# Kernel tuning notes

Hardware: AMD Instinct MI355X
Metric: run time of the kernel (lower is better)

The kernel has to match this reference:

```python
import jax, jax.numpy as jnp
import numpy as np

V, D, F, H, L = 32000, 1024, 4096, 16, 6
HD = D // H
EPS = 1e-5


def _posenc(S):
    pos = jnp.arange(S, dtype=jnp.float32)[:, None]
    div = jnp.exp(jnp.arange(0, D, 2, dtype=jnp.float32) * (-jnp.log(10000.0) / D))
    enc = jnp.zeros((S, D), jnp.float32)
    enc = enc.at[:, 0::2].set(jnp.sin(pos * div))
    enc = enc.at[:, 1::2].set(jnp.cos(pos * div))
    return enc


def _mha(xq, xkv, Wq, bq, Wk, bk, Wv, bv, Wo, bo, causal):
    B, Sq, _ = xq.shape
    Sk = xkv.shape[1]
    q = (xq @ Wq.T + bq).reshape(B, Sq, H, HD)
    k = (xkv @ Wk.T + bk).reshape(B, Sk, H, HD)
    v = (xkv @ Wv.T + bv).reshape(B, Sk, H, HD)
    scores = jnp.einsum('bqhd,bkhd->bhqk', q, k) / jnp.sqrt(jnp.float32(HD))
    if causal:
        mask = jnp.tril(jnp.ones((Sq, Sk), dtype=bool))
        scores = jnp.where(mask, scores, -jnp.inf)
    w = jax.nn.softmax(scores, axis=-1)
    out = jnp.einsum('bhqk,bkhd->bqhd', w, v).reshape(B, Sq, D)
    return out @ Wo.T + bo


def _ln(x, g, b):
    mu = jnp.mean(x, axis=-1, keepdims=True)
    var = jnp.mean((x - mu) ** 2, axis=-1, keepdims=True)
    return (x - mu) / jnp.sqrt(var + EPS) * g + b


def setup_inputs() -> dict:
    key = jax.random.key(0)
    ks = jax.random.split(key, 32)
    B, S, Se = 4, 512, 512
    s = 0.02
    inp = {
        'text': jax.random.randint(ks[0], (B, S), 0, V),
        'encoder_output': jax.random.normal(ks[1], (B, Se, D), jnp.float32),
        'W_e': jax.random.normal(ks[2], (V, D), jnp.float32) * s,
        'b_out': jnp.zeros((V,), jnp.float32),
        'ln_g': jnp.ones((D,), jnp.float32),
        'ln_b': jnp.zeros((D,), jnp.float32),
        'W1': jax.random.normal(ks[3], (F, D), jnp.float32) * s,
        'b1': jnp.zeros((F,), jnp.float32),
        'W2': jax.random.normal(ks[4], (D, F), jnp.float32) * s,
        'b2': jnp.zeros((D,), jnp.float32),
    }
    names = ['mWq', 'mWk', 'mWv', 'mWo', 'cWq', 'cWk', 'cWv', 'cWo']
    for i, n in enumerate(names):
        inp[n] = jax.random.normal(ks[5 + i], (D, D), jnp.float32) * s
        inp[n.replace('W', 'b')] = jnp.zeros((D,), jnp.float32)
    return inp


def reference(text, encoder_output, W_e, b_out, ln_g, ln_b, W1, b1, W2, b2,
              mWq, mbq, mWk, mbk, mWv, mbv, mWo, mbo,
              cWq, cbq, cWk, cbk, cWv, cbv, cWo, cbo):
    # embed + sinusoidal positional encoding (dropout is identity in eval)
    x = W_e[text] + _posenc(text.shape[1])[None, :, :]
    # NOTE: the torch module reuses the SAME attention/FFN/LN weights each layer
    for _ in range(L):
        a = _ln(x + _mha(x, x, mWq, mbq, mWk, mbk, mWv, mbv, mWo, mbo, True), ln_g, ln_b)
        c = _ln(_mha(a, encoder_output, cWq, cbq, cWk, cbk, cWv, cbv, cWo, cbo, False) + a, ln_g, ln_b)
        f = jax.nn.relu(c @ W1.T + b1) @ W2.T + b2
        x = _ln(c + f, ln_g, ln_b)
    logits = x @ W_e.T + b_out  # tied embedding weights
    # nn.Softmax() with dim=None on a 3-D tensor -> torch legacy dim=0
    return jax.nn.softmax(logits, axis=0)
```

## Files before the change

kernel.cpp:

```cpp
#include <hip/hip_runtime.h>

#define D_MODEL 1024
#define SEQ     512
#define NBATCH  4
#define NHEAD   16
#define HDIM    64
#define NTOK    2048
#define VOCAB   32000
#define FFDIM   4096
#define MiB     (1024*1024)

typedef _Float16 f16;
typedef f16   f16x8 __attribute__((ext_vector_type(8)));
typedef float f32x4 __attribute__((ext_vector_type(4)));

__device__ __forceinline__ void async_cp16(f16* lds, const f16* g) {
    __builtin_amdgcn_global_load_lds(
        (const __attribute__((address_space(1))) unsigned int*)g,
        (__attribute__((address_space(3))) unsigned int*)lds, 16, 0, 0);
}

__device__ __forceinline__ float block_sum(float v, float* lds) {
    #pragma unroll
    for (int o = 1; o < 64; o <<= 1) v += __shfl_xor(v, o);
    int w = threadIdx.x >> 6;
    if ((threadIdx.x & 63) == 0) lds[w] = v;
    __syncthreads();
    v = lds[0] + lds[1] + lds[2] + lds[3];
    __syncthreads();
    return v;
}

__global__ __launch_bounds__(256) void f32_to_f16_kernel(
    const float* __restrict__ in, f16* __restrict__ out, int n)
{
    int i0 = blockIdx.x * 1024 + threadIdx.x;
    #pragma unroll
    for (int e = 0; e < 4; e++) {
        int i = i0 + e * 256;
        if (i < n) out[i] = (f16)in[i];
    }
}

__global__ __launch_bounds__(256) void embed_kernel(
    const int* __restrict__ text, const float* __restrict__ We,
    float* __restrict__ X, f16* __restrict__ X16)
{
    int s = blockIdx.x;
    int tid = threadIdx.x;
    int tok[NBATCH];
    #pragma unroll
    for (int b = 0; b < NBATCH; b++) tok[b] = text[b * SEQ + s];
    const float kf = 9.210340371976184f / 1024.f;
    #pragma unroll
    for (int e = 0; e < 4; e++) {
        int d = tid + e * 256;
        int i2 = d & ~1;
        float freq = expf(-(float)i2 * kf);
        float ang = (float)s * freq;
        float pe = (d & 1) ? cosf(ang) : sinf(ang);
        #pragma unroll
        for (int b = 0; b < NBATCH; b++) {
            float v = We[(size_t)tok[b] * D_MODEL + d] + pe;
            size_t off = (size_t)(b * SEQ + s) * D_MODEL + d;
            X[off] = v;
            X16[off] = (f16)v;
        }
    }
}

template<bool RELU, int OUTMODE, int BM, bool QKV3>
__global__ __launch_bounds__(256) void gemm16_kernel(
    const f16* __restrict__ A, const f16* __restrict__ W,
    const float* __restrict__ bias, const float* __restrict__ bias2,
    const float* __restrict__ bias3,
    float* __restrict__ C, f16* __restrict__ C16, int M, int N, int K)
{
    constexpr int AM = BM / 2;
    constexpr int TM = AM / 16;
    __shared__ __align__(16) f16 As[BM * 32];
    __shared__ __align__(16) f16 Bs[128 * 32];
    const int tid  = threadIdx.x;
    const int lane = tid & 63;
    const int wv   = tid >> 6;
    const int wr   = (wv >> 1) * AM;
    const int wc   = (wv & 1) * 64;
    const int m0 = blockIdx.y * BM;
    const int n0 = blockIdx.x * 128;
    const int lm = lane & 15;
    const int lk = (lane >> 4) * 8;

    f32x4 acc[TM][4] = {};

    for (int k0 = 0; k0 < K; k0 += 32) {
        #pragma unroll
        for (int e = 0; e < BM / 64; e++) {
            int s = tid + e * 256;
            int row = s >> 2, cb = s & 3;
            async_cp16(&As[s * 8], &A[(size_t)(m0 + row) * K + k0 + cb * 8]);
        }
        #pragma unroll
        for (int e = 0; e < 2; e++) {
            int s = tid + e * 256;
            int row = s >> 2, cb = s & 3;
            async_cp16(&Bs[s * 8], &W[(size_t)(n0 + row) * K + k0 + cb * 8]);
        }
        __syncthreads();
        f16x8 af[TM], bfr[4];
        #pragma unroll
        for (int i = 0; i < TM; i++)
            af[i]  = *(const f16x8*)&As[(wr + i * 16 + lm) * 32 + lk];
        #pragma unroll
        for (int j = 0; j < 4; j++)
            bfr[j] = *(const f16x8*)&Bs[(wc + j * 16 + lm) * 32 + lk];
        #pragma unroll
        for (int i = 0; i < TM; i++)
            #pragma unroll
            for (int j = 0; j < 4; j++)
                acc[i][j] = __builtin_amdgcn_mfma_f32_16x16x32_f16(
                    af[i], bfr[j], acc[i][j], 0, 0, 0);
        __syncthreads();
    }

    const int rq = (lane >> 4) * 4;
    #pragma unroll
    for (int i = 0; i < TM; i++) {
        #pragma unroll
        for (int j = 0; j < 4; j++) {
            int col = n0 + wc + j * 16 + lm;
            float bj;
            if (QKV3) {
                const float* bp = col < 1024 ? bias : (col < 2048 ? bias2 : bias3);
                bj = bp[col & 1023];
            } else {
                bj = bias[col];
            }
            if (OUTMODE == 2) {
                int srow = (m0 + wr + i * 16 + rq) >> 2;
                float v[4];
                float mx = -1e30f;
                #pragma unroll
                for (int r = 0; r < 4; r++) {
                    v[r] = acc[i][j][r] + bj;
                    mx = fmaxf(mx, v[r]);
                }
                float ssum = 0.f;
                #pragma unroll
                for (int r = 0; r < 4; r++) { v[r] = expf(v[r] - mx); ssum += v[r]; }
                float inv = 1.f / ssum;
                #pragma unroll
                for (int r = 0; r < 4; r++)
                    C[((size_t)r * SEQ + srow) * N + col] = v[r] * inv;
            } else {
                #pragma unroll
                for (int r = 0; r < 4; r++) {
                    int row = m0 + wr + i * 16 + rq + r;
                    float v = acc[i][j][r] + bj;
                    if (RELU) v = fmaxf(v, 0.f);
                    if (OUTMODE == 0) C[(size_t)row * N + col] = v;
                    else              C16[(size_t)row * N + col] = (f16)v;
                }
            }
        }
    }
}

template<int CAUSAL>
__global__ __launch_bounds__(256) void attn_sm_kernel(
    const f16* __restrict__ Qb, const f16* __restrict__ Kb,
    f16* __restrict__ P, int ldq, int ldk, int qoff, int koff)
{
    __shared__ __align__(16) f16 Qs[2][64][32];
    __shared__ __align__(16) f16 Ks[2][2][128][32];
    const int bh = blockIdx.y;
    const int b = bh >> 4, h = bh & 15;
    const int q0 = blockIdx.x * 64;
    const int tid  = threadIdx.x;
    const int lane = tid & 63;
    const int w    = tid >> 6;
    const int lm   = lane & 15;
    const int lk   = (lane >> 4) * 8;
    const int nkt  = CAUSAL ? (q0 >> 7) + 1 : 4;
    const int nj   = nkt * 8;

    const f16* Qg = Qb + (size_t)(b * SEQ + q0) * ldq + qoff + h * HDIM;
    const f16* Kg = Kb + (size_t)(b * SEQ) * ldk + koff + h * HDIM;

    #pragma unroll
    for (int e = 0; e < 2; e++) {
        int cc = tid + e * 256;
        int ks = cc >> 8, row = (cc >> 2) & 63, cb = cc & 3;
        async_cp16(&Qs[ks][row][cb * 8], &Qg[(size_t)row * ldq + ks * 32 + cb * 8]);
    }
    #pragma unroll
    for (int e = 0; e < 4; e++) {
        int cc = tid + e * 256;
        int ks = cc >> 9, row = (cc >> 2) & 127, cb = cc & 3;
        async_cp16(&Ks[0][ks][row][cb * 8], &Kg[(size_t)row * ldk + ks * 32 + cb * 8]);
    }
    __syncthreads();

    f16x8 af[2];
    af[0] = *(const f16x8*)&Qs[0][w * 16 + lm][lk];
    af[1] = *(const f16x8*)&Qs[1][w * 16 + lm][lk];

    f32x4 acc[32] = {};

    #pragma unroll
    for (int kt = 0; kt < 4; kt++) {
        if (kt < nkt) {
            if (kt + 1 < nkt) {
                const f16* src = Kg + (size_t)(kt + 1) * 128 * ldk;
                int buf = (kt + 1) & 1;
                #pragma unroll
                for (int e = 0; e < 4; e++) {
                    int cc = tid + e * 256;
                    int ks = cc >> 9, row = (cc >> 2) & 127, cb = cc & 3;
                    async_cp16(&Ks[buf][ks][row][cb * 8],
                               &src[(size_t)row * ldk + ks * 32 + cb * 8]);
                }
            }
            #pragma unroll
            for (int ks = 0; ks < 2; ks++)
                #pragma unroll
                for (int j = 0; j < 8; j++) {
                    f16x8 bf = *(const f16x8*)&Ks[kt & 1][ks][j * 16 + lm][lk];
                    acc[kt * 8 + j] = __builtin_amdgcn_mfma_f32_16x16x32_f16(
                        af[ks], bf, acc[kt * 8 + j], 0, 0, 0);
                }
            if (kt + 1 < nkt) __syncthreads();
        }
    }

    const int rq = (lane >> 4) * 4;
    #pragma unroll
    for (int r = 0; r < 4; r++) {
        const int qq = q0 + w * 16 + rq + r;
        float mr = -1e30f;
        #pragma unroll
        for (int j = 0; j < 32; j++) {
            if (j < nj) {
                float v = acc[j][r] * 0.125f;
                if (CAUSAL && (j * 16 + lm) > qq) v = -1e30f;
                acc[j][r] = v;
                mr = fmaxf(mr, v);
            }
        }
        mr = fmaxf(mr, __shfl_xor(mr, 1));
        mr = fmaxf(mr, __shfl_xor(mr, 2));
        mr = fmaxf(mr, __shfl_xor(mr, 4));
        mr = fmaxf(mr, __shfl_xor(mr, 8));
        float sum = 0.f;
        #pragma unroll
        for (int j = 0; j < 32; j++) {
            if (j < nj) {
                float e = expf(acc[j][r] - mr);
                acc[j][r] = e;
                sum += e;
            }
        }
        sum += __shfl_xor(sum, 1);
        sum += __shfl_xor(sum, 2);
        sum += __shfl_xor(sum, 4);
        sum += __shfl_xor(sum, 8);
        float inv = 1.f / sum;
        f16* prow = P + ((size_t)bh * SEQ + qq) * SEQ + lm;
        #pragma unroll
        for (int j = 0; j < 32; j++) {
            float pv = (j < nj) ? acc[j][r] * inv : 0.f;
            prow[j * 16] = (f16)pv;
        }
    }
}

__global__ __launch_bounds__(256) void attn_av16_kernel(
    const f16* __restrict__ P, const f16* __restrict__ Vt,
    f16* __restrict__ O16, int causal)
{
    __shared__ __align__(16) f16 Ps[64 * 32];
    __shared__ __align__(16) f16 Vs[64 * 32];
    const int bh = blockIdx.y;
    const int b = bh >> 4, h = bh & 15;
    const int q0 = blockIdx.x * 64;
    const int tid  = threadIdx.x;
    const int lane = tid & 63;
    const int wv   = tid >> 6;
    const int wr   = (wv >> 1) * 32;
    const int wc   = (wv & 1) * 32;
    const int lm   = lane & 15;
    const int lk   = (lane >> 4) * 8;
    const f16* Pg = P  + ((size_t)bh * SEQ + q0) * SEQ;
    const f16* Vg = Vt + (size_t)bh * HDIM * SEQ;
    const int klim = causal ? q0 + 64 : SEQ;

    f32x4 acc[2][2] = {};
    for (int k0 = 0; k0 < klim; k0 += 32) {
        int row = tid >> 2, cb = tid & 3;
        async_cp16(&Ps[tid * 8], &Pg[(size_t)row * SEQ + k0 + cb * 8]);
        async_cp16(&Vs[tid * 8], &Vg[(size_t)row * SEQ + k0 + cb * 8]);
        __syncthreads();
        f16x8 af[2], bf[2];
        #pragma unroll
        for (int i = 0; i < 2; i++)
            af[i] = *(const f16x8*)&Ps[(wr + i * 16 + lm) * 32 + lk];
        #pragma unroll
        for (int j = 0; j < 2; j++)
            bf[j] = *(const f16x8*)&Vs[(wc + j * 16 + lm) * 32 + lk];
        #pragma unroll
        for (int i = 0; i < 2; i++)
            #pragma unroll
            for (int j = 0; j < 2; j++)
                acc[i][j] = __builtin_amdgcn_mfma_f32_16x16x32_f16(
                    af[i], bf[j], acc[i][j], 0, 0, 0);
        __syncthreads();
    }

    const int rq = (lane >> 4) * 4;
    #pragma unroll
    for (int i = 0; i < 2; i++)
        #pragma unroll
        for (int j = 0; j < 2; j++)
            #pragma unroll
            for (int r = 0; r < 4; r++)
                O16[(size_t)(b * SEQ + q0 + wr + i * 16 + rq + r) * D_MODEL
                    + h * HDIM + wc + j * 16 + lm] = (f16)acc[i][j][r];
}

__global__ __launch_bounds__(256) void vtrans_kernel(
    const f16* __restrict__ V, f16* __restrict__ Vt, int ldv, int vbase)
{
    __shared__ __align__(16) f16 t[64][72];
    const int bh = blockIdx.y;
    const int b = bh >> 4, h = bh & 15;
    const int s0 = blockIdx.x * 64;
    const int tid = threadIdx.x;
    const int r = tid >> 3;
    const int c8 = (tid & 7) * 8;
    #pragma unroll
    for (int half = 0; half < 2; half++) {
        int row = r + half * 32;
        f16x8 v = *(const f16x8*)&V[(size_t)(b * SEQ + s0 + row) * ldv
                                    + vbase + h * HDIM + c8];
        #pragma unroll
        for (int j = 0; j < 8; j++) t[c8 + j][row] = v[j];
    }
    __syncthreads();
    const int d = tid >> 2;
    const int sblk = (tid & 3) * 16;
    f16* dst = Vt + ((size_t)bh * HDIM + d) * SEQ + s0 + sblk;
    *(f16x8*)&dst[0] = *(const f16x8*)&t[d][sblk];
    *(f16x8*)&dst[8] = *(const f16x8*)&t[d][sblk + 8];
}

template<bool IL>
__global__ __launch_bounds__(256) void add_ln_kernel(
    const float* __restrict__ X, const float* __restrict__ Y,
    const float* __restrict__ g, const float* __restrict__ bb,
    float* __restrict__ Out, f16* __restrict__ Out16)
{
    __shared__ float lds[4];
    int row = blockIdx.x;
    const float* xp = X + (size_t)row * D_MODEL;
    const float* yp = Y + (size_t)row * D_MODEL;
    int tid = threadIdx.x;
    float s[4];
    float lsum = 0.f;
    #pragma unroll
    for (int e = 0; e < 4; e++) {
        int d = tid + e * 256;
        s[e] = xp[d] + yp[d];
        lsum += s[e];
    }
    float mu = block_sum(lsum, lds) * (1.f / D_MODEL);
    float lv = 0.f;
    #pragma unroll
    for (int e = 0; e < 4; e++) { float t = s[e] - mu; lv += t * t; }
    float rstd = rsqrtf(block_sum(lv, lds) * (1.f / D_MODEL) + 1e-5f);
    int orow = IL ? ((row & (SEQ - 1)) * 4 + (row >> 9)) : row;
    #pragma unroll
    for (int e = 0; e < 4; e++) {
        int d = tid + e * 256;
        float v = (s[e] - mu) * rstd * g[d] + bb[d];
        Out[(size_t)row * D_MODEL + d] = v;
        Out16[(size_t)orow * D_MODEL + d] = (f16)v;
    }
}

extern "C" void kernel_launch(void* const* d_in, const int* in_sizes, int n_in,
                              void* d_out, int out_size, void* d_ws, size_t ws_size,
                              hipStream_t stream)
{
    const int*   text = (const int*)d_in[0];
    const float* enc  = (const float*)d_in[1];
    const float* W_e  = (const float*)d_in[2];
    const float* b_out= (const float*)d_in[3];
    const float* ln_g = (const float*)d_in[4];
    const float* ln_b = (const float*)d_in[5];
    const float* W1   = (const float*)d_in[6];
    const float* b1   = (const float*)d_in[7];
    const float* W2   = (const float*)d_in[8];
    const float* b2   = (const float*)d_in[9];
    const float* mWq  = (const float*)d_in[10]; const float* mbq = (const float*)d_in[11];
    const float* mWk  = (const float*)d_in[12]; const float* mbk = (const float*)d_in[13];
    const float* mWv  = (const float*)d_in[14]; const float* mbv = (const float*)d_in[15];
    const float* mWo  = (const float*)d_in[16]; const float* mbo = (const float*)d_in[17];
    const float* cWq  = (const float*)d_in[18]; const float* cbq = (const float*)d_in[19];
    const float* cWk  = (const float*)d_in[20]; const float* cbk = (const float*)d_in[21];
    const float* cWv  = (const float*)d_in[22]; const float* cbv = (const float*)d_in[23];
    const float* cWo  = (const float*)d_in[24]; const float* cbo = (const float*)d_in[25];
    float* out = (float*)d_out;

    char* w8 = (char*)d_ws;
    float* x    = (float*)(w8 +   0 * (size_t)MiB);
    float* a    = (float*)(w8 +   8 * (size_t)MiB);
    float* c    = (float*)(w8 +  16 * (size_t)MiB);
    float* o    = (float*)(w8 +  80 * (size_t)MiB);
    char* scratch = w8 + 88 * (size_t)MiB;
    f16* P16    = (f16*)scratch;
    f16* ffh16  = (f16*)scratch;
    f16* cWk16s = (f16*)scratch;
    f16* cWv16s = (f16*)(scratch + 2 * (size_t)MiB);
    f16* enc16  = (f16*)(scratch + 4 * (size_t)MiB);
    f16* qkv16  = (f16*)(w8 + 120 * (size_t)MiB);
    f16* q16    = qkv16;
    f16* vt16   = (f16*)(w8 + 132 * (size_t)MiB);
    f16* enck16 = (f16*)(w8 + 136 * (size_t)MiB);
    f16* encvt16= (f16*)(w8 + 140 * (size_t)MiB);
    f16* attn16 = (f16*)(w8 + 144 * (size_t)MiB);
    f16* x16    = (f16*)(w8 + 148 * (size_t)MiB);
    f16* a16    = (f16*)(w8 + 152 * (size_t)MiB);
    f16* c16    = (f16*)(w8 + 156 * (size_t)MiB);
    f16* mQKV16 = (f16*)(w8 + 160 * (size_t)MiB);
    f16* mWo16  = (f16*)(w8 + 166 * (size_t)MiB);
    f16* cWq16  = (f16*)(w8 + 168 * (size_t)MiB);
    f16* cWo16  = (f16*)(w8 + 170 * (size_t)MiB);
    f16* W116   = (f16*)(w8 + 172 * (size_t)MiB);
    f16* W216   = (f16*)(w8 + 180 * (size_t)MiB);
    f16* We16   = (f16*)(w8 + 188 * (size_t)MiB);

    auto conv = [&](const float* src, f16* dst, int n) {
        f32_to_f16_kernel<<<(n + 1023) / 1024, 256, 0, stream>>>(src, dst, n);
    };

    const int DD = D_MODEL * D_MODEL;
    conv(mWq, mQKV16, DD);
    conv(mWk, mQKV16 + (size_t)DD, DD);
    conv(mWv, mQKV16 + 2 * (size_t)DD, DD);
    conv(mWo, mWo16, DD);
    conv(cWq, cWq16, DD); conv(cWk, cWk16s, DD); conv(cWv, cWv16s, DD); conv(cWo, cWo16, DD);
    conv(W1, W116, FFDIM * D_MODEL); conv(W2, W216, FFDIM * D_MODEL);
    conv(W_e, We16, VOCAB * D_MODEL);
    conv(enc, enc16, NTOK * D_MODEL);

    embed_kernel<<<SEQ, 256, 0, stream>>>(text, W_e, x, x16);

    gemm16_kernel<false, 1, 64, false><<<dim3(D_MODEL / 128, NTOK / 64), 256, 0, stream>>>(
        enc16, cWk16s, cbk, nullptr, nullptr, nullptr, enck16, NTOK, D_MODEL, D_MODEL);
    gemm16_kernel<false, 1, 64, false><<<dim3(D_MODEL / 128, NTOK / 64), 256, 0, stream>>>(
        enc16, cWv16s, cbv, nullptr, nullptr, nullptr, attn16, NTOK, D_MODEL, D_MODEL);
    vtrans_kernel<<<dim3(SEQ / 64, NBATCH * NHEAD), 256, 0, stream>>>(
        attn16, encvt16, D_MODEL, 0);

    const int BH = NBATCH * NHEAD;
    for (int layer = 0; layer < 6; layer++) {
        gemm16_kernel<false, 1, 64, true><<<dim3(3072 / 128, NTOK / 64), 256, 0, stream>>>(
            x16, mQKV16, mbq, mbk, mbv, nullptr, qkv16, NTOK, 3072, D_MODEL);
        vtrans_kernel<<<dim3(SEQ / 64, BH), 256, 0, stream>>>(qkv16, vt16, 3072, 2048);
        attn_sm_kernel<1><<<dim3(SEQ / 64, BH), 256, 0, stream>>>(
            qkv16, qkv16, P16, 3072, 3072, 0, 1024);
        attn_av16_kernel<<<dim3(SEQ / 64, BH), 256, 0, stream>>>(P16, vt16, attn16, 1);
        gemm16_kernel<false, 0, 64, false><<<dim3(D_MODEL / 128, NTOK / 64), 256, 0, stream>>>(
            attn16, mWo16, mbo, nullptr, nullptr, o, nullptr, NTOK, D_MODEL, D_MODEL);
        add_ln_kernel<false><<<NTOK, 256, 0, stream>>>(x, o, ln_g, ln_b, a, a16);

        gemm16_kernel<false, 1, 64, false><<<dim3(D_MODEL / 128, NTOK / 64), 256, 0, stream>>>(
            a16, cWq16, cbq, nullptr, nullptr, nullptr, q16, NTOK, D_MODEL, D_MODEL);
        attn_sm_kernel<0><<<dim3(SEQ / 64, BH), 256, 0, stream>>>(
            q16, enck16, P16, D_MODEL, D_MODEL, 0, 0);
        attn_av16_kernel<<<dim3(SEQ / 64, BH), 256, 0, stream>>>(P16, encvt16, attn16, 0);
        gemm16_kernel<false, 0, 64, false><<<dim3(D_MODEL / 128, NTOK / 64), 256, 0, stream>>>(
            attn16, cWo16, cbo, nullptr, nullptr, o, nullptr, NTOK, D_MODEL, D_MODEL);
        add_ln_kernel<false><<<NTOK, 256, 0, stream>>>(o, a, ln_g, ln_b, c, c16);

        gemm16_kernel<true, 1, 128, false><<<dim3(FFDIM / 128, NTOK / 128), 256, 0, stream>>>(
            c16, W116, b1, nullptr, nullptr, nullptr, ffh16, NTOK, FFDIM, D_MODEL);
        gemm16_kernel<false, 0, 64, false><<<dim3(D_MODEL / 128, NTOK / 64), 256, 0, stream>>>(
            ffh16, W216, b2, nullptr, nullptr, o, nullptr, NTOK, D_MODEL, FFDIM);
        if (layer < 5)
            add_ln_kernel<false><<<NTOK, 256, 0, stream>>>(c, o, ln_g, ln_b, x, x16);
        else
            add_ln_kernel<true><<<NTOK, 256, 0, stream>>>(c, o, ln_g, ln_b, x, x16);
    }

    gemm16_kernel<false, 2, 128, false><<<dim3(VOCAB / 128, NTOK / 128), 256, 0, stream>>>(
        x16, We16, b_out, nullptr, nullptr, out, nullptr, NTOK, VOCAB, D_MODEL);
}
```

Before: 2.445 ms.

## Fuse attention softmax with PV product and widen GEMM K-tile with XOR swizzle

```diff
diff --git a/kernel.cpp b/kernel.cpp
--- a/kernel.cpp
+++ b/kernel.cpp
@@ -78,8 +78,8 @@
 {
     constexpr int AM = BM / 2;
     constexpr int TM = AM / 16;
-    __shared__ __align__(16) f16 As[BM * 32];
-    __shared__ __align__(16) f16 Bs[128 * 32];
+    __shared__ __align__(16) f16 As[BM * 64];
+    __shared__ __align__(16) f16 Bs[128 * 64];
     const int tid  = threadIdx.x;
     const int lane = tid & 63;
     const int wv   = tid >> 6;
@@ -88,41 +88,50 @@
     const int m0 = blockIdx.y * BM;
     const int n0 = blockIdx.x * 128;
     const int lm = lane & 15;
-    const int lk = (lane >> 4) * 8;
+    const int lg = lane >> 4;
 
     f32x4 acc[TM][4] = {};
 
-    for (int k0 = 0; k0 < K; k0 += 32) {
-        #pragma unroll
-        for (int e = 0; e < BM / 64; e++) {
+    for (int k0 = 0; k0 < K; k0 += 64) {
+        #pragma unroll
+        for (int e = 0; e < BM / 32; e++) {
             int s = tid + e * 256;
-            int row = s >> 2, cb = s & 3;
-            async_cp16(&As[s * 8], &A[(size_t)(m0 + row) * K + k0 + cb * 8]);
-        }
-        #pragma unroll
-        for (int e = 0; e < 2; e++) {
+            int row = s >> 3, cb = s & 7;
+            async_cp16(&As[s * 8],
+                       &A[(size_t)(m0 + row) * K + k0 + ((cb ^ (row & 7)) * 8)]);
+        }
+        #pragma unroll
+        for (int e = 0; e < 4; e++) {
             int s = tid + e * 256;
-            int row = s >> 2, cb = s & 3;
-            async_cp16(&Bs[s * 8], &W[(size_t)(n0 + row) * K + k0 + cb * 8]);
+            int row = s >> 3, cb = s & 7;
+            async_cp16(&Bs[s * 8],
+                       &W[(size_t)(n0 + row) * K + k0 + ((cb ^ (row & 7)) * 8)]);
         }
         __syncthreads();
-        f16x8 af[TM], bfr[4];
-        #pragma unroll
-        for (int i = 0; i < TM; i++)
-            af[i]  = *(const f16x8*)&As[(wr + i * 16 + lm) * 32 + lk];
-        #pragma unroll
-        for (int j = 0; j < 4; j++)
-            bfr[j] = *(const f16x8*)&Bs[(wc + j * 16 + lm) * 32 + lk];
-        #pragma unroll
-        for (int i = 0; i < TM; i++)
+        #pragma unroll
+        for (int ks = 0; ks < 2; ks++) {
+            f16x8 af[TM], bfr[4];
             #pragma unroll
-            for (int j = 0; j < 4; j++)
-                acc[i][j] = __builtin_amdgcn_mfma_f32_16x16x32_f16(
-                    af[i], bfr[j], acc[i][j], 0, 0, 0);
+            for (int i = 0; i < TM; i++) {
+                int arow = wr + i * 16 + lm;
+                af[i] = *(const f16x8*)&As[arow * 64 + (((ks * 4 + lg) ^ (arow & 7)) * 8)];
+            }
+            #pragma unroll
+            for (int j = 0; j < 4; j++) {
+                int brow = wc + j * 16 + lm;
+                bfr[j] = *(const f16x8*)&Bs[brow * 64 + (((ks * 4 + lg) ^ (brow & 7)) * 8)];
+            }
+            #pragma unroll
+            for (int i = 0; i < TM; i++)
+                #pragma unroll
+                for (int j = 0; j < 4; j++)
+                    acc[i][j] = __builtin_amdgcn_mfma_f32_16x16x32_f16(
+                        af[i], bfr[j], acc[i][j], 0, 0, 0);
+        }
         __syncthreads();
     }
 
-    const int rq = (lane >> 4) * 4;
+    const int rq = lg * 4;
     #pragma unroll
     for (int i = 0; i < TM; i++) {
         #pragma unroll
@@ -166,12 +175,16 @@
 }
 
 template<int CAUSAL>
-__global__ __launch_bounds__(256) void attn_sm_kernel(
+__global__ __launch_bounds__(256, 1) void attn_fused_kernel(
     const f16* __restrict__ Qb, const f16* __restrict__ Kb,
-    f16* __restrict__ P, int ldq, int ldk, int qoff, int koff)
-{
-    __shared__ __align__(16) f16 Qs[2][64][32];
-    __shared__ __align__(16) f16 Ks[2][2][128][32];
+    const f16* __restrict__ Vt, f16* __restrict__ O16,
+    int ldq, int ldk, int qoff, int koff)
+{
+    __shared__ __align__(16) char smem[114688];
+    f16* QV = (f16*)smem;
+    f16* Ks = (f16*)(smem + 16384);
+    f16* Ps = (f16*)(smem + 49152);
+
     const int bh = blockIdx.y;
     const int b = bh >> 4, h = bh & 15;
     const int q0 = blockIdx.x * 64;
@@ -179,30 +192,33 @@
     const int lane = tid & 63;
     const int w    = tid >> 6;
     const int lm   = lane & 15;
-    const int lk   = (lane >> 4) * 8;
+    const int lg   = lane >> 4;
     const int nkt  = CAUSAL ? (q0 >> 7) + 1 : 4;
-    const int nj   = nkt * 8;
 
     const f16* Qg = Qb + (size_t)(b * SEQ + q0) * ldq + qoff + h * HDIM;
     const f16* Kg = Kb + (size_t)(b * SEQ) * ldk + koff + h * HDIM;
+    const f16* Vg = Vt + (size_t)bh * HDIM * SEQ;
 
     #pragma unroll
     for (int e = 0; e < 2; e++) {
-        int cc = tid + e * 256;
-        int ks = cc >> 8, row = (cc >> 2) & 63, cb = cc & 3;
-        async_cp16(&Qs[ks][row][cb * 8], &Qg[(size_t)row * ldq + ks * 32 + cb * 8]);
+        int s = tid + e * 256;
+        int row = s >> 3, cb = s & 7;
+        async_cp16(&QV[s * 8], &Qg[(size_t)row * ldq + ((cb ^ (row & 7)) * 8)]);
     }
     #pragma unroll
     for (int e = 0; e < 4; e++) {
-        int cc = tid + e * 256;
-        int ks = cc >> 9, row = (cc >> 2) & 127, cb = cc & 3;
-        async_cp16(&Ks[0][ks][row][cb * 8], &Kg[(size_t)row * ldk + ks * 32 + cb * 8]);
+        int s = tid + e * 256;
+        int row = s >> 3, cb = s & 7;
+        async_cp16(&Ks[s * 8], &Kg[(size_t)row * ldk + ((cb ^ (row & 7)) * 8)]);
     }
     __syncthreads();
 
     f16x8 af[2];
-    af[0] = *(const f16x8*)&Qs[0][w * 16 + lm][lk];
-    af[1] = *(const f16x8*)&Qs[1][w * 16 + lm][lk];
+    {
+        int arow = w * 16 + lm;
+        af[0] = *(const f16x8*)&QV[arow * 64 + (((lg) ^ (arow & 7)) * 8)];
+        af[1] = *(const f16x8*)&QV[arow * 64 + (((4 + lg) ^ (arow & 7)) * 8)];
+    }
 
     f32x4 acc[32] = {};
 
@@ -211,20 +227,23 @@
         if (kt < nkt) {
             if (kt + 1 < nkt) {
                 const f16* src = Kg + (size_t)(kt + 1) * 128 * ldk;
-                int buf = (kt + 1) & 1;
+                f16* dst = &Ks[((kt + 1) & 1) * 8192];
                 #pragma unroll
                 for (int e = 0; e < 4; e++) {
-                    int cc = tid + e * 256;
-                    int ks = cc >> 9, row = (cc >> 2) & 127, cb = cc & 3;
-                    async_cp16(&Ks[buf][ks][row][cb * 8],
-                               &src[(size_t)row * ldk + ks * 32 + cb * 8]);
+                    int s = tid + e * 256;
+                    int row = s >> 3, cb = s & 7;
+                    async_cp16(&dst[s * 8],
+                               &src[(size_t)row * ldk + ((cb ^ (row & 7)) * 8)]);
                 }
             }
+            const f16* kb = &Ks[(kt & 1) * 8192];
             #pragma unroll
             for (int ks = 0; ks < 2; ks++)
                 #pragma unroll
                 for (int j = 0; j < 8; j++) {
-                    f16x8 bf = *(const f16x8*)&Ks[kt & 1][ks][j * 16 + lm][lk];
+                    int brow = j * 16 + lm;
+                    f16x8 bf = *(const f16x8*)&kb[brow * 64 +
+                                    (((ks * 4 + lg) ^ (brow & 7)) * 8)];
                     acc[kt * 8 + j] = __builtin_amdgcn_mfma_f32_16x16x32_f16(
                         af[ks], bf, acc[kt * 8 + j], 0, 0, 0);
                 }
@@ -232,10 +251,12 @@
         }
     }
 
-    const int rq = (lane >> 4) * 4;
+    const int nj = nkt * 8;
+    const int rq = lg * 4;
     #pragma unroll
     for (int r = 0; r < 4; r++) {
-        const int qq = q0 + w * 16 + rq + r;
+        const int ql = w * 16 + rq + r;
+        const int qq = q0 + ql;
         float mr = -1e30f;
         #pragma unroll
         for (int j = 0; j < 32; j++) {
@@ -264,66 +285,63 @@
         sum += __shfl_xor(sum, 4);
         sum += __shfl_xor(sum, 8);
         float inv = 1.f / sum;
-        f16* prow = P + ((size_t)bh * SEQ + qq) * SEQ + lm;
         #pragma unroll
         for (int j = 0; j < 32; j++) {
-            float pv = (j < nj) ? acc[j][r] * inv : 0.f;
-            prow[j * 16] = (f16)pv;
-        }
-    }
-}
-
-__global__ __launch_bounds__(256) void attn_av16_kernel(
-    const f16* __restrict__ P, const f16* __restrict__ Vt,
-    f16* __restrict__ O16, int causal)
-{
-    __shared__ __align__(16) f16 Ps[64 * 32];
-    __shared__ __align__(16) f16 Vs[64 * 32];
-    const int bh = blockIdx.y;
-    const int b = bh >> 4, h = bh & 15;
-    const int q0 = blockIdx.x * 64;
-    const int tid  = threadIdx.x;
-    const int lane = tid & 63;
-    const int wv   = tid >> 6;
-    const int wr   = (wv >> 1) * 32;
-    const int wc   = (wv & 1) * 32;
-    const int lm   = lane & 15;
-    const int lk   = (lane >> 4) * 8;
-    const f16* Pg = P  + ((size_t)bh * SEQ + q0) * SEQ;
-    const f16* Vg = Vt + (size_t)bh * HDIM * SEQ;
-    const int klim = causal ? q0 + 64 : SEQ;
-
-    f32x4 acc[2][2] = {};
-    for (int k0 = 0; k0 < klim; k0 += 32) {
-        int row = tid >> 2, cb = tid & 3;
-        async_cp16(&Ps[tid * 8], &Pg[(size_t)row * SEQ + k0 + cb * 8]);
-        async_cp16(&Vs[tid * 8], &Vg[(size_t)row * SEQ + k0 + cb * 8]);
-        __syncthreads();
-        f16x8 af[2], bf[2];
-        #pragma unroll
-        for (int i = 0; i < 2; i++)
-            af[i] = *(const f16x8*)&Ps[(wr + i * 16 + lm) * 32 + lk];
-        #pragma unroll
-        for (int j = 0; j < 2; j++)
-            bf[j] = *(const f16x8*)&Vs[(wc + j * 16 + lm) * 32 + lk];
-        #pragma unroll
-        for (int i = 0; i < 2; i++)
+            if (j < nj) {
+                int k = j * 16 + lm;
+                int cs = (k >> 3) ^ (ql & 7);
+                Ps[ql * 512 + cs * 8 + (k & 7)] = (f16)(acc[j][r] * inv);
+            }
+        }
+    }
+
+    __syncthreads();
+    const int nvt = CAUSAL ? nkt * 2 : 8;
+    #pragma unroll
+    for (int e = 0; e < 2; e++) {
+        int s = tid + e * 256;
+        int row = s >> 3, cb = s & 7;
+        async_cp16(&QV[s * 8], &Vg[(size_t)row * SEQ + ((cb ^ (row & 7)) * 8)]);
+    }
+    __syncthreads();
+
+    f32x4 acc_o[4] = {};
+    const int qlr = w * 16 + lm;
+    for (int t = 0; t < nvt; t++) {
+        if (t + 1 < nvt) {
+            const f16* src = Vg + (t + 1) * 64;
+            f16* dst = &QV[((t + 1) & 1) * 4096];
             #pragma unroll
-            for (int j = 0; j < 2; j++)
-                acc[i][j] = __builtin_amdgcn_mfma_f32_16x16x32_f16(
-                    af[i], bf[j], acc[i][j], 0, 0, 0);
-        __syncthreads();
-    }
-
-    const int rq = (lane >> 4) * 4;
-    #pragma unroll
-    for (int i = 0; i < 2; i++)
-        #pragma unroll
-        for (int j = 0; j < 2; j++)
+            for (int e = 0; e < 2; e++) {
+                int s = tid + e * 256;
+                int row = s >> 3, cb = s & 7;
+                async_cp16(&dst[s * 8],
+                           &src[(size_t)row * SEQ + ((cb ^ (row & 7)) * 8)]);
+            }
+        }
+        const f16* vb = &QV[(t & 1) * 4096];
+        #pragma unroll
+        for (int ks = 0; ks < 2; ks++) {
+            int ck = t * 8 + ks * 4 + lg;
+            f16x8 ap = *(const f16x8*)&Ps[qlr * 512 + ((ck ^ (qlr & 7)) * 8)];
             #pragma unroll
-            for (int r = 0; r < 4; r++)
-                O16[(size_t)(b * SEQ + q0 + wr + i * 16 + rq + r) * D_MODEL
-                    + h * HDIM + wc + j * 16 + lm] = (f16)acc[i][j][r];
+            for (int jd = 0; jd < 4; jd++) {
+                int vrow = jd * 16 + lm;
+                f16x8 bf = *(const f16x8*)&vb[vrow * 64 +
+                                (((ks * 4 + lg) ^ (vrow & 7)) * 8)];
+                acc_o[jd] = __builtin_amdgcn_mfma_f32_16x16x32_f16(
+                    ap, bf, acc_o[jd], 0, 0, 0);
+            }
+        }
+        if (t + 1 < nvt) __syncthreads();
+    }
+
+    #pragma unroll
+    for (int jd = 0; jd < 4; jd++)
+        #pragma unroll
+        for (int r = 0; r < 4; r++)
+            O16[(size_t)(b * SEQ + q0 + w * 16 + rq + r) * D_MODEL
+                + h * HDIM + jd * 16 + lm] = (f16)acc_o[jd][r];
 }
 
 __global__ __launch_bounds__(256) void vtrans_kernel(
@@ -416,7 +434,6 @@
     float* c    = (float*)(w8 +  16 * (size_t)MiB);
     float* o    = (float*)(w8 +  80 * (size_t)MiB);
     char* scratch = w8 + 88 * (size_t)MiB;
-    f16* P16    = (f16*)scratch;
     f16* ffh16  = (f16*)scratch;
     f16* cWk16s = (f16*)scratch;
     f16* cWv16s = (f16*)(scratch + 2 * (size_t)MiB);
@@ -466,18 +483,16 @@
         gemm16_kernel<false, 1, 64, true><<<dim3(3072 / 128, NTOK / 64), 256, 0, stream>>>(
             x16, mQKV16, mbq, mbk, mbv, nullptr, qkv16, NTOK, 3072, D_MODEL);
         vtrans_kernel<<<dim3(SEQ / 64, BH), 256, 0, stream>>>(qkv16, vt16, 3072, 2048);
-        attn_sm_kernel<1><<<dim3(SEQ / 64, BH), 256, 0, stream>>>(
-            qkv16, qkv16, P16, 3072, 3072, 0, 1024);
-        attn_av16_kernel<<<dim3(SEQ / 64, BH), 256, 0, stream>>>(P16, vt16, attn16, 1);
+        attn_fused_kernel<1><<<dim3(SEQ / 64, BH), 256, 0, stream>>>(
+            qkv16, qkv16, vt16, attn16, 3072, 3072, 0, 1024);
         gemm16_kernel<false, 0, 64, false><<<dim3(D_MODEL / 128, NTOK / 64), 256, 0, stream>>>(
             attn16, mWo16, mbo, nullptr, nullptr, o, nullptr, NTOK, D_MODEL, D_MODEL);
         add_ln_kernel<false><<<NTOK, 256, 0, stream>>>(x, o, ln_g, ln_b, a, a16);
 
         gemm16_kernel<false, 1, 64, false><<<dim3(D_MODEL / 128, NTOK / 64), 256, 0, stream>>>(
             a16, cWq16, cbq, nullptr, nullptr, nullptr, q16, NTOK, D_MODEL, D_MODEL);
-        attn_sm_kernel<0><<<dim3(SEQ / 64, BH), 256, 0, stream>>>(
-            q16, enck16, P16, D_MODEL, D_MODEL, 0, 0);
-        attn_av16_kernel<<<dim3(SEQ / 64, BH), 256, 0, stream>>>(P16, encvt16, attn16, 0);
+        attn_fused_kernel<0><<<dim3(SEQ / 64, BH), 256, 0, stream>>>(
+            q16, enck16, encvt16, attn16, D_MODEL, D_MODEL, 0, 0);
         gemm16_kernel<false, 0, 64, false><<<dim3(D_MODEL / 128, NTOK / 64), 256, 0, stream>>>(
             attn16, cWo16, cbo, nullptr, nullptr, o, nullptr, NTOK, D_MODEL, D_MODEL);
         add_ln_kernel<false><<<NTOK, 256, 0, stream>>>(o, a, ln_g, ln_b, c, c16);
```

Result: faster. 2.282 ms (-6.7%).
